# Kernel tuning notes

Measured on AMD Instinct MI355X. Metric: run time of the kernel, lower is better.

Reference implementation:

```python
import jax, jax.numpy as jnp
import numpy as np

B, S, N_ITEMS, E, H, L, DFF = 32, 512, 2048, 512, 8, 2, 2048
DK = E // H
EPS = 1e-5


def setup_inputs() -> dict:
    key = jax.random.key(0)
    ks = jax.random.split(key, 32)
    sc = 0.02
    p = {
        'input_seq': jax.random.normal(ks[0], (B, S, N_ITEMS), jnp.float32),
        'emb_W': jax.random.normal(ks[1], (N_ITEMS, E), jnp.float32) * sc,
        'emb_b': jnp.zeros((E,), jnp.float32),
        'pos_emb': jax.random.normal(ks[2], (S, E), jnp.float32) * sc,
        'Wq': jax.random.normal(ks[3], (L, E, E), jnp.float32) * sc,
        'bq': jnp.zeros((L, E), jnp.float32),
        'Wk': jax.random.normal(ks[4], (L, E, E), jnp.float32) * sc,
        'bk': jnp.zeros((L, E), jnp.float32),
        'Wv': jax.random.normal(ks[5], (L, E, E), jnp.float32) * sc,
        'bv': jnp.zeros((L, E), jnp.float32),
        'Wo': jax.random.normal(ks[6], (L, E, E), jnp.float32) * sc,
        'bo': jnp.zeros((L, E), jnp.float32),
        'ln1_g': jnp.ones((L, E), jnp.float32),
        'ln1_b': jnp.zeros((L, E), jnp.float32),
        'W1': jax.random.normal(ks[7], (L, E, DFF), jnp.float32) * sc,
        'b1': jnp.zeros((L, DFF), jnp.float32),
        'W2': jax.random.normal(ks[8], (L, DFF, E), jnp.float32) * sc,
        'b2': jnp.zeros((L, E), jnp.float32),
        'ln2_g': jnp.ones((L, E), jnp.float32),
        'ln2_b': jnp.zeros((L, E), jnp.float32),
        'fc_W': jax.random.normal(ks[9], (E, 1), jnp.float32) * sc,
        'fc_b': jnp.zeros((1,), jnp.float32),
    }
    return p


def _layernorm(x, g, b):
    m = jnp.mean(x, axis=-1, keepdims=True)
    v = jnp.mean(jnp.square(x - m), axis=-1, keepdims=True)
    return (x - m) * jax.lax.rsqrt(v + EPS) * g + b


def reference(input_seq, emb_W, emb_b, pos_emb, Wq, bq, Wk, bk, Wv, bv, Wo, bo,
              ln1_g, ln1_b, W1, b1, W2, b2, ln2_g, ln2_b, fc_W, fc_b):
    x = input_seq @ emb_W + emb_b          # [B,S,E]
    x = x + pos_emb[None, :, :]
    tril = jnp.tril(jnp.ones((S, S), jnp.float32))  # causal lower-triangular
    for l in range(L):
        # --- self attention (faithful: tril BEFORE scale, zeros not -inf) ---
        q = (x @ Wq[l] + bq[l]).reshape(B, S, H, DK).transpose(0, 2, 1, 3)
        k = (x @ Wk[l] + bk[l]).reshape(B, S, H, DK).transpose(0, 2, 1, 3)
        v = (x @ Wv[l] + bv[l]).reshape(B, S, H, DK).transpose(0, 2, 1, 3)
        scores = jnp.einsum('bhqd,bhkd->bhqk', q, k)
        scores = (scores * tril) / np.sqrt(DK)
        probs = jax.nn.softmax(scores, axis=-1)
        attn = jnp.einsum('bhqk,bhkd->bhqd', probs, v)  # [B,H,S,DK]
        attn = attn.transpose(0, 2, 1, 3).reshape(B, S, E)
        attn = attn @ Wo[l] + bo[l]
        # faithful source bug: `self_attention(x,x,x)[0]` -> batch 0 only,
        # broadcast over all batches in the residual add
        attended0 = attn[0]                 # [S,E]
        x = _layernorm(x + attended0[None, :, :], ln1_g[l], ln1_b[l])
        # --- feed forward ---
        ff = jax.nn.relu(x @ W1[l] + b1[l]) @ W2[l] + b2[l]
        x = _layernorm(x + ff, ln2_g[l], ln2_b[l])
    out = (x @ fc_W + fc_b).squeeze(-1)     # [B,S]
    return out
```

## Files before the change

kernel.cpp:

```cpp
#include <hip/hip_runtime.h>


typedef __bf16 bf16;
typedef __bf16 bf16x8 __attribute__((ext_vector_type(8)));
typedef __bf16 bf16x4 __attribute__((ext_vector_type(4)));
typedef float  f32x4  __attribute__((ext_vector_type(4)));

#define SEQ 512

__device__ __forceinline__ void gl2lds16(const bf16* g, void* l) {
    __builtin_amdgcn_global_load_lds(
        (const __attribute__((address_space(1))) void*)g,
        (__attribute__((address_space(3))) void*)l, 16, 0, 0);
}

template<int N> __device__ __forceinline__ void waitvm() {
    if constexpr (N == 0) asm volatile("s_waitcnt vmcnt(0)" ::: "memory");
    else if constexpr (N == 2) asm volatile("s_waitcnt vmcnt(2)" ::: "memory");
    else if constexpr (N == 4) asm volatile("s_waitcnt vmcnt(4)" ::: "memory");
    else if constexpr (N == 8) asm volatile("s_waitcnt vmcnt(8)" ::: "memory");
    else static_assert(N == 0, "unsupported waitvm");
}

template<int BM, int BN, int ACT, int POS, int WPE>
__global__ __launch_bounds__(512, WPE)
void mgemm2(const bf16* __restrict__ Ab, int lda,
            const bf16* __restrict__ Bt, int ldb,
            const float* __restrict__ bias, const float* __restrict__ pos,
            bf16* __restrict__ Cb, int ldc, int K)
{
    constexpr int WN = (BN >= 256 ? 4 : 2);
    constexpr int WM = 8 / WN;
    constexpr int RPW = BM / WM;
    constexpr int MR = RPW / 16;
    constexpr int NR = 4;
    constexpr int ABY = BM * 64;
    constexpr int BBY = BN * 64;
    constexpr int APASS = BM / 128;
    constexpr int BPASS = BN / 128;
    constexpr int OPT = APASS + BPASS;
    constexpr int NBUF = 4;
    __shared__ __align__(1024) char smem[NBUF * (ABY + BBY)];
    char* AsB = smem;
    char* BsB = smem + NBUF * ABY;

    const int gx = gridDim.x, gy = gridDim.y;
    const int nwg = gx * gy;
    const int b = blockIdx.y * gx + blockIdx.x;
    const int q = nwg >> 3, r = nwg & 7;
    const int xcd = b & 7, loc = b >> 3;
    const int wg = (xcd < r ? xcd * (q + 1) : r * (q + 1) + (xcd - r) * q) + loc;
    const int bx = wg % gx, by = wg / gx;
    const int row0 = by * BM, col0 = bx * BN;

    const int tid = threadIdx.x;
    const int lane = tid & 63;
    const int wv = tid >> 6;
    const int wr = wv / WN, wc = wv % WN;
    const int fr = lane & 15, fc = lane >> 4;

    const bf16* aS[APASS];
    #pragma unroll
    for (int p = 0; p < APASS; ++p) {
        int cL = p * 512 + tid;
        int row = cL >> 2, ch = cL & 3;
        aS[p] = Ab + (long long)(row0 + row) * lda + ((ch ^ (row & 3)) * 8);
    }
    const bf16* bS[BPASS];
    #pragma unroll
    for (int p = 0; p < BPASS; ++p) {
        int cL = p * 512 + tid;
        int row = cL >> 2, ch = cL & 3;
        bS[p] = Bt + (long long)(col0 + row) * ldb + ((ch ^ (row & 3)) * 8);
    }
    int aOff[MR], bOff[NR];
    #pragma unroll
    for (int m = 0; m < MR; ++m) {
        int row = wr * RPW + m * 16 + fr;
        aOff[m] = row * 64 + ((fc ^ (row & 3)) * 16);
    }
    #pragma unroll
    for (int n = 0; n < NR; ++n) {
        int row = wc * 64 + n * 16 + fr;
        bOff[n] = row * 64 + ((fc ^ (row & 3)) * 16);
    }

    auto stage = [&](int buf, int kt) {
        #pragma unroll
        for (int p = 0; p < APASS; ++p)
            gl2lds16(aS[p] + kt, AsB + buf * ABY + (p * 512 + tid) * 16);
        #pragma unroll
        for (int p = 0; p < BPASS; ++p)
            gl2lds16(bS[p] + kt, BsB + buf * BBY + (p * 512 + tid) * 16);
    };

    f32x4 acc[MR][NR] = {};
    const int nt = K >> 5;

    stage(0, 0);
    if (nt > 1) stage(1, 32);
    if (nt > 2) stage(2, 64);

    for (int t = 0; t < nt; ++t) {
        const int staged = (t + 3 < nt ? t + 3 : nt);
        const int allow = (staged - t - 1) * OPT;
        if (allow >= 2 * OPT)      waitvm<2 * OPT>();
        else if (allow >= OPT)     waitvm<OPT>();
        else                       waitvm<0>();
        __builtin_amdgcn_s_barrier();
        if (t + 3 < nt) stage((t + 3) & 3, (t + 3) * 32);

        const int cur = t & 3;
        bf16x8 a[MR], b2[NR];
        #pragma unroll
        for (int m = 0; m < MR; ++m)
            a[m] = *(const bf16x8*)(AsB + cur * ABY + aOff[m]);
        #pragma unroll
        for (int n = 0; n < NR; ++n)
            b2[n] = *(const bf16x8*)(BsB + cur * BBY + bOff[n]);
        __builtin_amdgcn_s_setprio(1);
        #pragma unroll
        for (int m = 0; m < MR; ++m)
            #pragma unroll
            for (int n = 0; n < NR; ++n)
                acc[m][n] = __builtin_amdgcn_mfma_f32_16x16x32_bf16(
                    a[m], b2[n], acc[m][n], 0, 0, 0);
        __builtin_amdgcn_s_setprio(0);
    }

    __builtin_amdgcn_s_barrier();
    float* st = (float*)(smem + wv * 4096);
    const int rowb = row0 + wr * RPW;
    const int colb = col0 + wc * 64;
    #pragma unroll
    for (int m = 0; m < MR; ++m) {
        #pragma unroll
        for (int n = 0; n < NR; ++n) {
            int col = colb + n * 16 + fr;
            float bb = bias ? bias[col] : 0.f;
            #pragma unroll
            for (int rr = 0; rr < 4; ++rr) {
                float x = acc[m][n][rr] + bb;
                if constexpr (POS) {
                    int rowg = rowb + m * 16 + fc * 4 + rr;
                    x += pos[(rowg & 511) * 512 + col];
                }
                if constexpr (ACT) x = fmaxf(x, 0.f);
                st[(fc * 4 + rr) * 64 + n * 16 + fr] = x;
            }
        }
        #pragma unroll
        for (int s = 0; s < 2; ++s) {
            int row = s * 8 + (lane >> 3);
            int c8 = (lane & 7) * 8;
            f32x4 u = *(const f32x4*)&st[row * 64 + c8];
            f32x4 v = *(const f32x4*)&st[row * 64 + c8 + 4];
            bf16x8 w8;
            w8[0] = (bf16)u[0]; w8[1] = (bf16)u[1];
            w8[2] = (bf16)u[2]; w8[3] = (bf16)u[3];
            w8[4] = (bf16)v[0]; w8[5] = (bf16)v[1];
            w8[6] = (bf16)v[2]; w8[7] = (bf16)v[3];
            *(bf16x8*)&Cb[(long long)(rowb + m * 16 + row) * ldc + colb + c8] = w8;
        }
    }
}

template<int BM, int BN, int ACT, int CMODE, int CAUSAL>
__global__ __launch_bounds__(256, 4)
void mgemm(const bf16* __restrict__ Ab, int lda, long long sA,
           const bf16* __restrict__ Bt, int ldb, long long sB,
           const float* __restrict__ bias,
           float* __restrict__ Cf, bf16* __restrict__ Cb, int ldc, long long sC,
           int K)
{
    static_assert(BM == 128 && (BN == 128 || BN == 64), "tile");
    const int gx = gridDim.x, gy = gridDim.y;
    const int nwg = gx * gy;
    const int b = blockIdx.y * gx + blockIdx.x;
    const int q = nwg >> 3, r = nwg & 7;
    const int xcd = b & 7, loc = b >> 3;
    const int wg = (xcd < r ? xcd * (q + 1) : r * (q + 1) + (xcd - r) * q) + loc;
    const int bx = wg % gx, by = wg / gx;
    if (CAUSAL && bx * BN > by * BM + (BM - 1)) return;

    constexpr int TM = BM / 32, TN = BN / 32;
    constexpr int AIT = BM / 64, BIT = BN / 64;
    constexpr int ABY = BM * 64;
    constexpr int BBY = BN * 64;
    __shared__ bf16 As[2 * BM * 32];
    __shared__ bf16 Bs[2 * BN * 32];
    char* AsB = (char*)As;
    char* BsB = (char*)Bs;
    const int tid = threadIdx.x;
    const int lane = tid & 63, wv = tid >> 6;
    const int wr = wv >> 1, wc = wv & 1;
    const int fr = lane & 15, fc = lane >> 4;
    const int row0 = by * BM, col0 = bx * BN;
    const int z = blockIdx.z;

    Ab += (long long)z * sA;
    Bt += (long long)z * sB;
    if constexpr (CMODE == 0) Cf += (long long)z * sC;
    else                      Cb += (long long)z * sC;

    f32x4 acc[TM][TN] = {};

    const bf16* aSrc[AIT];
    #pragma unroll
    for (int it = 0; it < AIT; ++it) {
        int cL = it * 256 + tid;
        int row = cL >> 2, ch = cL & 3;
        aSrc[it] = Ab + (long long)(row0 + row) * lda + ((ch ^ (row & 3)) * 8);
    }
    const bf16* bSrc[BIT];
    #pragma unroll
    for (int it = 0; it < BIT; ++it) {
        int cL = it * 256 + tid;
        int row = cL >> 2, ch = cL & 3;
        bSrc[it] = Bt + (long long)(col0 + row) * ldb + ((ch ^ (row & 3)) * 8);
    }
    int aOff[TM], bOff[TN];
    #pragma unroll
    for (int m = 0; m < TM; ++m) {
        int row = wr * (BM / 2) + m * 16 + fr;
        aOff[m] = row * 64 + ((fc ^ (row & 3)) * 16);
    }
    #pragma unroll
    for (int n = 0; n < TN; ++n) {
        int row = wc * (BN / 2) + n * 16 + fr;
        bOff[n] = row * 64 + ((fc ^ (row & 3)) * 16);
    }

    auto stageTo = [&](int buf, int kt) {
        #pragma unroll
        for (int it = 0; it < AIT; ++it)
            gl2lds16(aSrc[it] + kt, AsB + buf * ABY + it * 4096 + wv * 1024);
        #pragma unroll
        for (int it = 0; it < BIT; ++it)
            gl2lds16(bSrc[it] + kt, BsB + buf * BBY + it * 4096 + wv * 1024);
    };

    const int nt = K >> 5;
    stageTo(0, 0);
    asm volatile("s_waitcnt vmcnt(0)" ::: "memory");
    __builtin_amdgcn_s_barrier();
    asm volatile("" ::: "memory");

    int cur = 0;
    for (int t = 0; t < nt; ++t) {
        if (t + 1 < nt) stageTo(cur ^ 1, (t + 1) * 32);
        bf16x8 a[TM], b2[TN];
        #pragma unroll
        for (int m = 0; m < TM; ++m) a[m] = *(const bf16x8*)(AsB + cur * ABY + aOff[m]);
        #pragma unroll
        for (int n = 0; n < TN; ++n) b2[n] = *(const bf16x8*)(BsB + cur * BBY + bOff[n]);
        __builtin_amdgcn_s_setprio(1);
        #pragma unroll
        for (int m = 0; m < TM; ++m)
            #pragma unroll
            for (int n = 0; n < TN; ++n)
                acc[m][n] = __builtin_amdgcn_mfma_f32_16x16x32_bf16(a[m], b2[n], acc[m][n], 0, 0, 0);
        __builtin_amdgcn_s_setprio(0);
        if (t + 1 < nt) {
            asm volatile("s_waitcnt vmcnt(0)" ::: "memory");
            __builtin_amdgcn_s_barrier();
            asm volatile("" ::: "memory");
            cur ^= 1;
        }
    }

    #pragma unroll
    for (int n = 0; n < TN; ++n) {
        int col = col0 + wc * (BN / 2) + n * 16 + fr;
        float bb = bias ? bias[col] : 0.f;
        #pragma unroll
        for (int m = 0; m < TM; ++m) {
            int rbase = row0 + wr * (BM / 2) + m * 16 + fc * 4;
            #pragma unroll
            for (int rr = 0; rr < 4; ++rr) {
                float x = acc[m][n][rr] + bb;
                if constexpr (ACT) x = fmaxf(x, 0.f);
                long long ci = (long long)(rbase + rr) * ldc + col;
                if constexpr (CMODE == 0) Cf[ci] = x;
                else                      Cb[ci] = (bf16)x;
            }
        }
    }
}

__global__ __launch_bounds__(256)
void cvt_k(const float* __restrict__ in, bf16* __restrict__ outb, long long n8)
{
    long long i = (long long)blockIdx.x * 256 + threadIdx.x;
    const long long stride = (long long)gridDim.x * 256;
    for (; i < n8; i += stride) {
        const float* p = in + i * 8;
        float4 u = *(const float4*)p;
        float4 v = *(const float4*)(p + 4);
        bf16x8 w8;
        w8[0] = (bf16)u.x; w8[1] = (bf16)u.y; w8[2] = (bf16)u.z; w8[3] = (bf16)u.w;
        w8[4] = (bf16)v.x; w8[5] = (bf16)v.y; w8[6] = (bf16)v.z; w8[7] = (bf16)v.w;
        *(bf16x8*)(outb + i * 8) = w8;
    }
}

__global__ __launch_bounds__(256)
void wt_k(const float* __restrict__ W, bf16* __restrict__ WT, int K, int N)
{
    __shared__ float t[32][33];
    int n0 = blockIdx.x * 32, k0 = blockIdx.y * 32;
    int r = threadIdx.x >> 3, c4 = (threadIdx.x & 7) * 4;
    float4 v = *(const float4*)&W[(long long)(k0 + r) * N + n0 + c4];
    t[r][c4 + 0] = v.x; t[r][c4 + 1] = v.y;
    t[r][c4 + 2] = v.z; t[r][c4 + 3] = v.w;
    __syncthreads();
    int n = threadIdx.x >> 3, kk4 = (threadIdx.x & 7) * 4;
    bf16x4 o;
    o[0] = (bf16)t[kk4 + 0][n]; o[1] = (bf16)t[kk4 + 1][n];
    o[2] = (bf16)t[kk4 + 2][n]; o[3] = (bf16)t[kk4 + 3][n];
    *(bf16x4*)&WT[(long long)(n0 + n) * K + k0 + kk4] = o;
}

__global__ __launch_bounds__(512)
void packb_k(const float* __restrict__ bq, const float* __restrict__ bk,
             const float* __restrict__ bv, float* __restrict__ dst)
{
    int l = blockIdx.x, t = threadIdx.x;
    dst[l * 1536 + t]        = bq[l * 512 + t];
    dst[l * 1536 + 512 + t]  = bk[l * 512 + t];
    dst[l * 1536 + 1024 + t] = bv[l * 512 + t];
}

__global__ __launch_bounds__(256)
void vt_k(const bf16* __restrict__ qkv, bf16* __restrict__ VT)
{
    __shared__ bf16 t[64][80];
    int h = blockIdx.y, s0 = blockIdx.x * 64;
    int r = threadIdx.x >> 2, c16 = (threadIdx.x & 3) * 16;
    const bf16* src = qkv + (long long)(s0 + r) * 1536 + 1024 + h * 64 + c16;
    *(bf16x8*)&t[r][c16]     = *(const bf16x8*)src;
    *(bf16x8*)&t[r][c16 + 8] = *(const bf16x8*)(src + 8);
    __syncthreads();
    int d = r, seg = c16;
    bf16 tmp[16];
    #pragma unroll
    for (int j = 0; j < 16; ++j) tmp[j] = t[seg + j][d];
    bf16* dst = VT + ((long long)(h * 64 + d)) * 512 + s0 + seg;
    *(bf16x8*)dst       = *(bf16x8*)&tmp[0];
    *(bf16x8*)(dst + 8) = *(bf16x8*)&tmp[8];
}

__global__ __launch_bounds__(256)
void softmax_k(const float* __restrict__ sc, bf16* __restrict__ pr)
{
    int row = blockIdx.x, h = blockIdx.y;
    const float* p = sc + ((long long)(h * SEQ + row)) * SEQ;
    bf16* o = pr + ((long long)(h * SEQ + row)) * SEQ;
    int tid = threadIdx.x;
    int j1 = tid + 256;
    float v0 = 0.f, v1 = 0.f;
    if (tid <= row) v0 = p[tid] * 0.125f;
    if (j1  <= row) v1 = p[j1]  * 0.125f;
    float m = fmaxf(v0, v1);
    #pragma unroll
    for (int off = 32; off; off >>= 1) m = fmaxf(m, __shfl_xor(m, off));
    __shared__ float red[4];
    if ((tid & 63) == 0) red[tid >> 6] = m;
    __syncthreads();
    m = fmaxf(fmaxf(red[0], red[1]), fmaxf(red[2], red[3]));
    float e0 = __expf(v0 - m);
    float e1 = __expf(v1 - m);
    float s = e0 + e1;
    #pragma unroll
    for (int off = 32; off; off >>= 1) s += __shfl_xor(s, off);
    __syncthreads();
    if ((tid & 63) == 0) red[tid >> 6] = s;
    __syncthreads();
    s = red[0] + red[1] + red[2] + red[3];
    float inv = 1.f / s;
    o[tid] = (bf16)(e0 * inv);
    o[j1]  = (bf16)(e1 * inv);
}

__global__ __launch_bounds__(128)
void addln_k(bf16* __restrict__ xb, const bf16* __restrict__ res,
             unsigned resMask, const float* __restrict__ g,
             const float* __restrict__ bta)
{
    long long row = blockIdx.x;
    int tid = threadIdx.x;
    int c = tid * 4;
    bf16x4 xv4 = *(const bf16x4*)&xb[row * 512 + c];
    bf16x4 rv4 = *(const bf16x4*)&res[(long long)(blockIdx.x & resMask) * 512 + c];
    float x0 = (float)xv4[0] + (float)rv4[0];
    float x1 = (float)xv4[1] + (float)rv4[1];
    float x2 = (float)xv4[2] + (float)rv4[2];
    float x3 = (float)xv4[3] + (float)rv4[3];
    float s = x0 + x1 + x2 + x3;
    float qq = x0 * x0 + x1 * x1 + x2 * x2 + x3 * x3;
    #pragma unroll
    for (int off = 32; off; off >>= 1) {
        s += __shfl_xor(s, off);
        qq += __shfl_xor(qq, off);
    }
    __shared__ float rs[2], rq[2];
    if ((tid & 63) == 0) { rs[tid >> 6] = s; rq[tid >> 6] = qq; }
    __syncthreads();
    s = rs[0] + rs[1]; qq = rq[0] + rq[1];
    float mean = s * (1.0f / 512.0f);
    float var  = qq * (1.0f / 512.0f) - mean * mean;
    float rstd = rsqrtf(var + 1e-5f);
    float4 gv = *(const float4*)&g[c];
    float4 bv = *(const float4*)&bta[c];
    bf16x4 o4;
    o4[0] = (bf16)((x0 - mean) * rstd * gv.x + bv.x);
    o4[1] = (bf16)((x1 - mean) * rstd * gv.y + bv.y);
    o4[2] = (bf16)((x2 - mean) * rstd * gv.z + bv.z);
    o4[3] = (bf16)((x3 - mean) * rstd * gv.w + bv.w);
    *(bf16x4*)&xb[row * 512 + c] = o4;
}

__global__ __launch_bounds__(256)
void fc_k(const bf16* __restrict__ x, const float* __restrict__ w,
          const float* __restrict__ bb, float* __restrict__ out)
{
    int row  = blockIdx.x * 4 + (threadIdx.x >> 6);
    int lane = threadIdx.x & 63;
    const bf16* xr = x + (long long)row * 512;
    bf16x8 a8 = *(const bf16x8*)&xr[lane * 8];
    float4 w0 = *(const float4*)&w[lane * 8];
    float4 w1 = *(const float4*)&w[lane * 8 + 4];
    float s = (float)a8[0] * w0.x + (float)a8[1] * w0.y
            + (float)a8[2] * w0.z + (float)a8[3] * w0.w
            + (float)a8[4] * w1.x + (float)a8[5] * w1.y
            + (float)a8[6] * w1.z + (float)a8[7] * w1.w;
    #pragma unroll
    for (int off = 32; off; off >>= 1) s += __shfl_xor(s, off);
    if (lane == 0) out[row] = s + bb[0];
}

extern "C" void kernel_launch(void* const* d_in, const int* in_sizes, int n_in,
                              void* d_out, int out_size, void* d_ws, size_t ws_size,
                              hipStream_t stream)
{
    const float* input_seq = (const float*)d_in[0];
    const float* emb_W  = (const float*)d_in[1];
    const float* emb_b  = (const float*)d_in[2];
    const float* pos_emb= (const float*)d_in[3];
    const float* Wq = (const float*)d_in[4];
    const float* bq = (const float*)d_in[5];
    const float* Wk = (const float*)d_in[6];
    const float* bk = (const float*)d_in[7];
    const float* Wv = (const float*)d_in[8];
    const float* bv = (const float*)d_in[9];
    const float* Wo = (const float*)d_in[10];
    const float* bo = (const float*)d_in[11];
    const float* ln1_g = (const float*)d_in[12];
    const float* ln1_b = (const float*)d_in[13];
    const float* W1 = (const float*)d_in[14];
    const float* b1 = (const float*)d_in[15];
    const float* W2 = (const float*)d_in[16];
    const float* b2 = (const float*)d_in[17];
    const float* ln2_g = (const float*)d_in[18];
    const float* ln2_b = (const float*)d_in[19];
    const float* fcW = (const float*)d_in[20];
    const float* fcb = (const float*)d_in[21];
    float* out = (float*)d_out;

    char* w = (char*)d_ws;
    size_t off = 0;
    auto alloc = [&](size_t bytes) -> void* {
        off = (off + 255) & ~(size_t)255;
        void* p = w + off;
        off += bytes;
        return p;
    };
    bf16*  xb     = (bf16*) alloc(16384ull * 512 * 2);
    bf16*  embWT  = (bf16*) alloc(512ull * 2048 * 2);
    bf16*  qkvWT  = (bf16*) alloc(2ull * 1536 * 512 * 2);
    bf16*  WoT    = (bf16*) alloc(2ull * 512 * 512 * 2);
    bf16*  W1T    = (bf16*) alloc(2ull * 2048 * 512 * 2);
    bf16*  W2T    = (bf16*) alloc(2ull * 512 * 2048 * 2);
    float* qkvB   = (float*)alloc(2ull * 1536 * 4);
    off = (off + 255) & ~(size_t)255;
    char* dynp = w + off;
    bf16*  seqb     = (bf16*)dynp;
    bf16*  qkv      = (bf16*)dynp;
    float* scores   = (float*)(dynp + 1572864);
    bf16*  probs    = (bf16*)(dynp + 1572864 + 8388608);
    bf16*  VT       = (bf16*)(dynp + 1572864 + 8388608 + 4194304);
    bf16*  attn0b   = (bf16*)(dynp + 1572864 + 8388608 + 4194304 + 524288);
    bf16*  attnout0b= (bf16*)(dynp + 1572864 + 8388608 + 4194304 + 524288 + 524288);
    bf16*  hidden = (bf16*)dynp;
    bf16*  ffout  = (bf16*)(dynp + 16384ull * 2048 * 2);

    dim3 blk(256);
    dim3 blk512(512);

    wt_k<<<dim3(16, 64), blk, 0, stream>>>(emb_W, embWT, 2048, 512);
    for (int l = 0; l < 2; ++l) {
        wt_k<<<dim3(16, 16), blk, 0, stream>>>(Wq + l * 262144, qkvWT + l * 786432,          512, 512);
        wt_k<<<dim3(16, 16), blk, 0, stream>>>(Wk + l * 262144, qkvWT + l * 786432 + 262144, 512, 512);
        wt_k<<<dim3(16, 16), blk, 0, stream>>>(Wv + l * 262144, qkvWT + l * 786432 + 524288, 512, 512);
        wt_k<<<dim3(16, 16), blk, 0, stream>>>(Wo + l * 262144, WoT + l * 262144, 512, 512);
        wt_k<<<dim3(64, 16), blk, 0, stream>>>(W1 + l * 1048576, W1T + l * 1048576, 512, 2048);
        wt_k<<<dim3(16, 64), blk, 0, stream>>>(W2 + l * 1048576, W2T + l * 1048576, 2048, 512);
    }
    packb_k<<<dim3(2), dim3(512), 0, stream>>>(bq, bk, bv, qkvB);
    cvt_k<<<dim3(2048), blk, 0, stream>>>(input_seq, seqb, 16384ll * 2048 / 8);

    mgemm2<128, 128, 0, 1, 4><<<dim3(4, 128), blk512, 0, stream>>>(
        seqb, 2048, embWT, 2048, emb_b, pos_emb, xb, 512, 2048);

    for (int l = 0; l < 2; ++l) {
        const bf16* qkvWT_l = qkvWT + l * 786432;
        const bf16* WoT_l   = WoT + l * 262144;
        const bf16* W1T_l   = W1T + l * 1048576;
        const bf16* W2T_l   = W2T + l * 1048576;

        mgemm<128, 128, 0, 1, 0><<<dim3(12, 4), blk, 0, stream>>>(
            xb, 512, 0, qkvWT_l, 512, 0, qkvB + l * 1536,
            nullptr, qkv, 1536, 0, 512);
        mgemm<128, 128, 0, 0, 1><<<dim3(4, 4, 8), blk, 0, stream>>>(
            qkv, 1536, 64, qkv + 512, 1536, 64, nullptr,
            scores, nullptr, 512, 262144, 64);
        softmax_k<<<dim3(512, 8), blk, 0, stream>>>(scores, probs);
        vt_k<<<dim3(8, 8), blk, 0, stream>>>(qkv, VT);
        mgemm<128, 64, 0, 1, 0><<<dim3(1, 4, 8), blk, 0, stream>>>(
            probs, 512, 262144, VT, 512, 32768, nullptr,
            nullptr, attn0b, 512, 64, 512);
        mgemm<128, 128, 0, 1, 0><<<dim3(4, 4), blk, 0, stream>>>(
            attn0b, 512, 0, WoT_l, 512, 0, bo + l * 512, nullptr,
            attnout0b, 512, 0, 512);
        addln_k<<<dim3(16384), dim3(128), 0, stream>>>(
            xb, attnout0b, 511u, ln1_g + l * 512, ln1_b + l * 512);

        mgemm2<256, 256, 1, 0, 2><<<dim3(8, 64), blk512, 0, stream>>>(
            xb, 512, W1T_l, 512, b1 + l * 2048, nullptr, hidden, 2048, 512);
        mgemm2<128, 128, 0, 0, 4><<<dim3(4, 128), blk512, 0, stream>>>(
            hidden, 2048, W2T_l, 2048, b2 + l * 512, nullptr, ffout, 512, 2048);
        addln_k<<<dim3(16384), dim3(128), 0, stream>>>(
            xb, ffout, 0xffffffffu, ln2_g + l * 512, ln2_b + l * 512);
    }

    fc_k<<<dim3(4096), blk, 0, stream>>>(xb, fcW, fcb, out);
}
```

Before: 433.9 us.

## Replace mgemm2 with 256-row tile GEMM using split-phase LDS prefetch pipeline

Replaces the big-GEMM kernel with a version fixed at BM=256 and one workgroup per CU. The K loop now works in 64-wide steps split into two 32-wide halves, with finer-grained staging of A and B parts issued after the LDS fragment reads. Waits and barriers are placed after the MFMAs so loads overlap compute better. Embedding and W2 GEMMs now use 256x128 tiles (half the grid), and W1 keeps 256x256, which lowers occupancy in exchange for more reuse per tile.

```diff
diff --git a/kernel.cpp b/kernel.cpp
--- a/kernel.cpp
+++ b/kernel.cpp
@@ -15,34 +15,34 @@
 }
 
 template<int N> __device__ __forceinline__ void waitvm() {
-    if constexpr (N == 0) asm volatile("s_waitcnt vmcnt(0)" ::: "memory");
+    if constexpr (N == 0)      asm volatile("s_waitcnt vmcnt(0)" ::: "memory");
     else if constexpr (N == 2) asm volatile("s_waitcnt vmcnt(2)" ::: "memory");
+    else if constexpr (N == 3) asm volatile("s_waitcnt vmcnt(3)" ::: "memory");
     else if constexpr (N == 4) asm volatile("s_waitcnt vmcnt(4)" ::: "memory");
+    else if constexpr (N == 5) asm volatile("s_waitcnt vmcnt(5)" ::: "memory");
+    else if constexpr (N == 6) asm volatile("s_waitcnt vmcnt(6)" ::: "memory");
     else if constexpr (N == 8) asm volatile("s_waitcnt vmcnt(8)" ::: "memory");
     else static_assert(N == 0, "unsupported waitvm");
 }
 
-template<int BM, int BN, int ACT, int POS, int WPE>
-__global__ __launch_bounds__(512, WPE)
-void mgemm2(const bf16* __restrict__ Ab, int lda,
-            const bf16* __restrict__ Bt, int ldb,
-            const float* __restrict__ bias, const float* __restrict__ pos,
-            bf16* __restrict__ Cb, int ldc, int K)
-{
-    constexpr int WN = (BN >= 256 ? 4 : 2);
-    constexpr int WM = 8 / WN;
-    constexpr int RPW = BM / WM;
-    constexpr int MR = RPW / 16;
-    constexpr int NR = 4;
-    constexpr int ABY = BM * 64;
-    constexpr int BBY = BN * 64;
-    constexpr int APASS = BM / 128;
+template<int BN, int ACT, int POS>
+__global__ __launch_bounds__(512, 1)
+void mg8(const bf16* __restrict__ Ab, int lda,
+         const bf16* __restrict__ Bt, int ldb,
+         const float* __restrict__ bias, const float* __restrict__ pos,
+         bf16* __restrict__ Cb, int ldc, int K)
+{
+    constexpr int BM = 256;
+    constexpr int APASS = 2;
     constexpr int BPASS = BN / 128;
-    constexpr int OPT = APASS + BPASS;
-    constexpr int NBUF = 4;
-    __shared__ __align__(1024) char smem[NBUF * (ABY + BBY)];
-    char* AsB = smem;
-    char* BsB = smem + NBUF * ABY;
+    constexpr int AHB = BM * 64;
+    constexpr int BHB = BN * 64;
+    constexpr int WM = (BN == 256 ? 2 : 4), WN = 8 / WM;
+    constexpr int MR = BM / WM / 16;
+    constexpr int NR = BN / WN / 16;
+    __shared__ __align__(1024) char smem[4 * AHB + 4 * BHB];
+    char* ABase = smem;
+    char* BBase = smem + 4 * AHB;
 
     const int gx = gridDim.x, gy = gridDim.y;
     const int nwg = gx * gy;
@@ -53,10 +53,9 @@
     const int bx = wg % gx, by = wg / gx;
     const int row0 = by * BM, col0 = bx * BN;
 
-    const int tid = threadIdx.x;
-    const int lane = tid & 63;
-    const int wv = tid >> 6;
-    const int wr = wv / WN, wc = wv % WN;
+    const int tid = threadIdx.x, lane = tid & 63, wv = tid >> 6;
+    const int wr = (WM == 2 ? (wv >> 2) : (wv >> 1));
+    const int wc = (WM == 2 ? (wv & 3) : (wv & 1));
     const int fr = lane & 15, fc = lane >> 4;
 
     const bf16* aS[APASS];
@@ -76,48 +75,58 @@
     int aOff[MR], bOff[NR];
     #pragma unroll
     for (int m = 0; m < MR; ++m) {
-        int row = wr * RPW + m * 16 + fr;
+        int row = wr * (BM / WM) + m * 16 + fr;
         aOff[m] = row * 64 + ((fc ^ (row & 3)) * 16);
     }
     #pragma unroll
     for (int n = 0; n < NR; ++n) {
-        int row = wc * 64 + n * 16 + fr;
+        int row = wc * (BN / WN) + n * 16 + fr;
         bOff[n] = row * 64 + ((fc ^ (row & 3)) * 16);
     }
 
-    auto stage = [&](int buf, int kt) {
-        #pragma unroll
-        for (int p = 0; p < APASS; ++p)
-            gl2lds16(aS[p] + kt, AsB + buf * ABY + (p * 512 + tid) * 16);
-        #pragma unroll
-        for (int p = 0; p < BPASS; ++p)
-            gl2lds16(bS[p] + kt, BsB + buf * BBY + (p * 512 + tid) * 16);
+    auto stagePart = [&](int j) {
+        const int tau = j >> 2, kh = (j >> 1) & 1, d = tau & 1;
+        const int koff = tau * 64 + kh * 32;
+        if (!(j & 1)) {
+            char* dst = ABase + (d * 2 + kh) * AHB + wv * 1024;
+            #pragma unroll
+            for (int p = 0; p < APASS; ++p)
+                gl2lds16(aS[p] + koff, dst + p * 8192);
+        } else {
+            char* dst = BBase + (d * 2 + kh) * BHB + wv * 1024;
+            #pragma unroll
+            for (int p = 0; p < BPASS; ++p)
+                gl2lds16(bS[p] + koff, dst + p * 8192);
+        }
     };
 
+    const int nt = K >> 6;
+    const int T = 4 * nt;
+    #pragma unroll
+    for (int j = 0; j < 6; ++j)
+        if (j < T) stagePart(j);
+    waitvm<2 * (APASS + BPASS)>();
+    __builtin_amdgcn_s_barrier();
+
     f32x4 acc[MR][NR] = {};
-    const int nt = K >> 5;
-
-    stage(0, 0);
-    if (nt > 1) stage(1, 32);
-    if (nt > 2) stage(2, 64);
-
-    for (int t = 0; t < nt; ++t) {
-        const int staged = (t + 3 < nt ? t + 3 : nt);
-        const int allow = (staged - t - 1) * OPT;
-        if (allow >= 2 * OPT)      waitvm<2 * OPT>();
-        else if (allow >= OPT)     waitvm<OPT>();
-        else                       waitvm<0>();
+    const int NPH = 2 * nt;
+    for (int g = 0; g < NPH; ++g) {
+        const int tau = g >> 1, ks = g & 1, d = tau & 1;
+
+        const char* as = ABase + (d * 2 + ks) * AHB;
+        const char* bs = BBase + (d * 2 + ks) * BHB;
+        bf16x8 a[MR], b2[NR];
+        #pragma unroll
+        for (int m = 0; m < MR; ++m) a[m] = *(const bf16x8*)(as + aOff[m]);
+        #pragma unroll
+        for (int n = 0; n < NR; ++n) b2[n] = *(const bf16x8*)(bs + bOff[n]);
+
+        if (2 * g + 6 < T) stagePart(2 * g + 6);
+        if (2 * g + 7 < T) stagePart(2 * g + 7);
+
         __builtin_amdgcn_s_barrier();
-        if (t + 3 < nt) stage((t + 3) & 3, (t + 3) * 32);
-
-        const int cur = t & 3;
-        bf16x8 a[MR], b2[NR];
-        #pragma unroll
-        for (int m = 0; m < MR; ++m)
-            a[m] = *(const bf16x8*)(AsB + cur * ABY + aOff[m]);
-        #pragma unroll
-        for (int n = 0; n < NR; ++n)
-            b2[n] = *(const bf16x8*)(BsB + cur * BBY + bOff[n]);
+        asm volatile("s_waitcnt lgkmcnt(0)" ::: "memory");
+        __builtin_amdgcn_sched_barrier(0);
         __builtin_amdgcn_s_setprio(1);
         #pragma unroll
         for (int m = 0; m < MR; ++m)
@@ -126,12 +135,19 @@
                 acc[m][n] = __builtin_amdgcn_mfma_f32_16x16x32_bf16(
                     a[m], b2[n], acc[m][n], 0, 0, 0);
         __builtin_amdgcn_s_setprio(0);
-    }
-
-    __builtin_amdgcn_s_barrier();
+
+        const int rem = T - (2 * g + 4);
+        if (rem >= 4)      waitvm<2 * (APASS + BPASS)>();
+        else if (rem == 3) waitvm<2 * APASS + BPASS>();
+        else if (rem == 2) waitvm<APASS + BPASS>();
+        else if (rem == 1) waitvm<APASS>();
+        else               waitvm<0>();
+        __builtin_amdgcn_s_barrier();
+    }
+
     float* st = (float*)(smem + wv * 4096);
-    const int rowb = row0 + wr * RPW;
-    const int colb = col0 + wc * 64;
+    const int rowb = row0 + wr * (BM / WM);
+    const int colb = col0 + wc * (BN / WN);
     #pragma unroll
     for (int m = 0; m < MR; ++m) {
         #pragma unroll
@@ -509,7 +525,7 @@
     packb_k<<<dim3(2), dim3(512), 0, stream>>>(bq, bk, bv, qkvB);
     cvt_k<<<dim3(2048), blk, 0, stream>>>(input_seq, seqb, 16384ll * 2048 / 8);
 
-    mgemm2<128, 128, 0, 1, 4><<<dim3(4, 128), blk512, 0, stream>>>(
+    mg8<128, 0, 1><<<dim3(4, 64), blk512, 0, stream>>>(
         seqb, 2048, embWT, 2048, emb_b, pos_emb, xb, 512, 2048);
 
     for (int l = 0; l < 2; ++l) {
@@ -535,9 +551,9 @@
         addln_k<<<dim3(16384), dim3(128), 0, stream>>>(
             xb, attnout0b, 511u, ln1_g + l * 512, ln1_b + l * 512);
 
-        mgemm2<256, 256, 1, 0, 2><<<dim3(8, 64), blk512, 0, stream>>>(
+        mg8<256, 1, 0><<<dim3(8, 64), blk512, 0, stream>>>(
             xb, 512, W1T_l, 512, b1 + l * 2048, nullptr, hidden, 2048, 512);
-        mgemm2<128, 128, 0, 0, 4><<<dim3(4, 128), blk512, 0, stream>>>(
+        mg8<128, 0, 0><<<dim3(4, 64), blk512, 0, stream>>>(
             hidden, 2048, W2T_l, 2048, b2 + l * 512, nullptr, ffout, 512, 2048);
         addln_k<<<dim3(16384), dim3(128), 0, stream>>>(
             xb, ffout, 0xffffffffu, ln2_g + l * 512, ln2_b + l * 512);
```

Result: no change. 441.3 us (median of 2 runs) (+1.7%).
